# Kernel tuning notes

Measured on AMD Instinct MI355X. Metric: run time of the kernel, lower is better.

The kernel has to match this reference:

```python
import jax, jax.numpy as jnp
import numpy as np

T_Q, T_K, B, H, V = 32, 48, 64, 1024, 32320
MASK_FILL = -65504.0  # GNMT uses fp16 min


def setup_inputs() -> dict:
    key = jax.random.key(0)
    ks = jax.random.split(key, 12)
    s = 0.02
    inp = {
        "input1": jax.random.normal(ks[0], (T_K, B, H), jnp.float32),
        "input0": jax.random.normal(ks[1], (T_K, B, H), jnp.float32),
        "input2": jax.random.randint(ks[2], (B,), 1, T_K + 1),          # context lengths in [1, T_K]
        "input3": jax.random.randint(ks[3], (T_Q, B), 0, V),            # decoder token ids
        "emb": (jax.random.normal(ks[4], (V, H), jnp.float32) * 0.1).at[0].set(0.0),  # padding_idx=0
        "W_ih": jax.random.normal(ks[5], (4 * H, H), jnp.float32) * s,
        "W_hh": jax.random.normal(ks[6], (4 * H, H), jnp.float32) * s,
        "b_ih": jnp.zeros((4 * H,), jnp.float32),
        "b_hh": jnp.zeros((4 * H,), jnp.float32),
        "W_q": jax.random.normal(ks[7], (H, H), jnp.float32) * s,
        "W_k": jax.random.normal(ks[8], (H, H), jnp.float32) * s,
        "v_att": jax.random.normal(ks[9], (H,), jnp.float32) * s,
        "norm_scalar": jnp.array([1.0 / np.sqrt(H)], jnp.float32),
        "norm_bias": jnp.zeros((H,), jnp.float32),
    }
    return inp


def _lstm(x, W_ih, W_hh, b_ih, b_hh):
    # x: (T, B, In). PyTorch LSTM gate order: i, f, g, o. Zero initial state.
    xp = jnp.einsum('tbi,gi->tbg', x, W_ih) + b_ih + b_hh  # (T, B, 4H)
    Hh = W_hh.shape[1]

    def step(carry, xt):
        h, c = carry
        gates = xt + h @ W_hh.T
        i, f, g, o = jnp.split(gates, 4, axis=-1)
        c = jax.nn.sigmoid(f) * c + jax.nn.sigmoid(i) * jnp.tanh(g)
        h = jax.nn.sigmoid(o) * jnp.tanh(c)
        return (h, c), h

    h0 = jnp.zeros((x.shape[1], Hh), x.dtype)
    _, hs = jax.lax.scan(step, (h0, h0), xp)
    return hs  # (T, B, H)


def _forward(input1, input0, input2, input3, emb, W_ih, W_hh, b_ih, b_hh,
             W_q, W_k, v_att, norm_scalar, norm_bias):
    x = emb[input3]                       # (T_Q, B, H) embedding lookup
    ctx = input0 + input1                 # (T_K, B, H) residual-summed encoder context
    rnn_out = _lstm(x, W_ih, W_hh, b_ih, b_hh)   # (T_Q, B, H)

    # Bahdanau attention (batch_first=False -> transpose to batch-first)
    q = rnn_out.transpose(1, 0, 2)        # (B, T_Q, H)
    keys = ctx.transpose(1, 0, 2)         # (B, T_K, H)
    aq = q @ W_q.T                        # (B, T_Q, H)
    ak = keys @ W_k.T                     # (B, T_K, H)
    v = v_att / jnp.linalg.norm(v_att) * norm_scalar[0]  # normalized attention vector
    sum_qk = aq[:, :, None, :] + ak[:, None, :, :] + norm_bias  # (B, T_Q, T_K, H)
    scores = jnp.einsum('bqkh,h->bqk', jnp.tanh(sum_qk), v)
    pad = jnp.arange(T_K)[None, :] >= input2[:, None]            # (B, T_K), True = pad
    scores = jnp.where(pad[:, None, :], MASK_FILL, scores)
    attn = jax.nn.softmax(scores, axis=-1)
    context = jnp.einsum('bqk,bkh->bqh', attn, keys).transpose(1, 0, 2)  # (T_Q, B, H)
    # dropout p=0 -> identity; returns (rnn_outputs, attn_context) = (out12, out11)
    return rnn_out, context


def reference(input1, input0, input2, input3, emb, W_ih, W_hh, b_ih, b_hh,
              W_q, W_k, v_att, norm_scalar, norm_bias):
    return _forward(input1, input0, input2, input3, emb, W_ih, W_hh, b_ih, b_hh,
                    W_q, W_k, v_att, norm_scalar, norm_bias)
```

## Files before the change

kernel.cpp:

```cpp
#include <hip/hip_runtime.h>
#include <hip/hip_bf16.h>

typedef unsigned short u16;
typedef __attribute__((ext_vector_type(8))) short bf16x8;
typedef __attribute__((ext_vector_type(8))) unsigned short us8;
typedef __attribute__((ext_vector_type(4))) float f32x4;

#define T_Q 32
#define T_K 48
#define NB 64
#define HDIM 1024
#define MASK_FILL -65504.0f
#define LSTM_BLOCKS 64

__device__ __forceinline__ float bf2f(u16 v){
  union { unsigned u; float f; } x; x.u = ((unsigned)v) << 16; return x.f;
}
__device__ __forceinline__ u16 f2bf(float f){
  union { float f; unsigned u; } x; x.f = f;
  return (u16)((x.u + 0x7FFFu + ((x.u >> 16) & 1u)) >> 16);
}
__device__ __forceinline__ float sigm(float x){
  return __builtin_amdgcn_rcpf(1.f + __expf(-x));
}
__device__ __forceinline__ float tanh_f(float x){
  float e = __expf(2.f * x);
  return fmaf(-2.f, __builtin_amdgcn_rcpf(e + 1.f), 1.f);
}

__device__ __forceinline__ void st_b32_cc(u16* a, unsigned v){
  asm volatile("global_store_dword %0, %1, off sc0 sc1" :: "v"(a), "v"(v) : "memory");
}
__device__ __forceinline__ void st_flag(int* a, int v){
  asm volatile("global_store_dword %0, %1, off sc0 sc1" :: "v"(a), "v"(v) : "memory");
}
__device__ __forceinline__ int ld_flag(const int* a){
  int r;
  asm volatile("global_load_dword %0, %1, off sc0 sc1\n\ts_waitcnt vmcnt(0)"
               : "=v"(r) : "v"(a) : "memory");
  return r;
}

#define MFMA16(A,B,C) __builtin_amdgcn_mfma_f32_16x16x32_bf16(A,B,C,0,0,0)


__global__ void conv_f2b(const float* __restrict__ s, u16* __restrict__ d){
  size_t i = ((size_t)blockIdx.x * 256 + threadIdx.x) * 4;
  float4 v = *(const float4*)(s + i);
  ushort4 o; o.x = f2bf(v.x); o.y = f2bf(v.y); o.z = f2bf(v.z); o.w = f2bf(v.w);
  *(ushort4*)(d + i) = o;
}

__global__ void gather_x(const int* __restrict__ tok, const float* __restrict__ emb,
                         u16* __restrict__ x){
  int r = blockIdx.x;
  int token = tok[r];
  float4 v = ((const float4*)(emb + (size_t)token * HDIM))[threadIdx.x];
  ushort4 o; o.x = f2bf(v.x); o.y = f2bf(v.y); o.z = f2bf(v.z); o.w = f2bf(v.w);
  ((ushort4*)(x + (size_t)r * HDIM))[threadIdx.x] = o;
}

__global__ void make_keys(const float* __restrict__ a, const float* __restrict__ b,
                          u16* __restrict__ o){
  size_t i = ((size_t)blockIdx.x * 256 + threadIdx.x) * 4;
  float4 va = *(const float4*)(a + i);
  float4 vb = *(const float4*)(b + i);
  ushort4 vo;
  vo.x = f2bf(va.x + vb.x);
  vo.y = f2bf(va.y + vb.y);
  vo.z = f2bf(va.z + vb.z);
  vo.w = f2bf(va.w + vb.w);
  *(ushort4*)(o + i) = vo;
}

__global__ void prep_small(const float* __restrict__ vatt, const float* __restrict__ ns,
                           const float* __restrict__ nb,
                           float* __restrict__ vhat, float* __restrict__ nbias){
  __shared__ float wred[4];
  int t = threadIdx.x, lane = t & 63, w = t >> 6;
  float vv[4]; float s = 0.f;
  #pragma unroll
  for (int j = 0; j < 4; j++){ vv[j] = vatt[t*4 + j]; s += vv[j]*vv[j]; }
  #pragma unroll
  for (int m = 32; m >= 1; m >>= 1) s += __shfl_xor(s, m);
  if (lane == 0) wred[w] = s;
  __syncthreads();
  float tot = wred[0] + wred[1] + wred[2] + wred[3];
  float scale = ns[0] / sqrtf(tot);
  #pragma unroll
  for (int j = 0; j < 4; j++) vhat[t*4 + j] = vv[j] * scale;
  #pragma unroll
  for (int j = 0; j < 4; j++){ int i = t + 256*j; nbias[i] = nb[i]; }
}

__global__ void prep_bsum(const float* __restrict__ bih, const float* __restrict__ bhh,
                          float* __restrict__ bias_sum){
  int i = blockIdx.x * 256 + threadIdx.x;
  bias_sum[i] = bih[i] + bhh[i];
}


template<int OB>
__global__ __launch_bounds__(256) void gemm_bf16(
  const u16* __restrict__ A, const u16* __restrict__ W,
  const float* __restrict__ bias, void* __restrict__ Cv,
  int M, int N, int K)
{
  __shared__ __align__(16) u16 As[4][66][8];
  __shared__ __align__(16) u16 Bs[4][66][8];
  const int t = threadIdx.x;
  const int m0 = blockIdx.y * 64, n0 = blockIdx.x * 64;
  const int lane = t & 63, w = t >> 6;
  const int wm = (w >> 1) * 32, wn = (w & 1) * 32;
  const int lr = lane & 15, g = lane >> 4;
  const int lrow = t >> 2, lkc = t & 3;
  f32x4 acc00 = {0,0,0,0}, acc01 = {0,0,0,0}, acc10 = {0,0,0,0}, acc11 = {0,0,0,0};
  const u16* aptr = A + (size_t)(m0 + lrow) * K + lkc * 8;
  const u16* wptr = W + (size_t)(n0 + lrow) * K + lkc * 8;
  for (int k0 = 0; k0 < K; k0 += 32){
    *(bf16x8*)(&As[lkc][lrow][0]) = *(const bf16x8*)(aptr + k0);
    *(bf16x8*)(&Bs[lkc][lrow][0]) = *(const bf16x8*)(wptr + k0);
    __syncthreads();
    bf16x8 a0 = *(const bf16x8*)(&As[g][wm      + lr][0]);
    bf16x8 a1 = *(const bf16x8*)(&As[g][wm + 16 + lr][0]);
    bf16x8 b0 = *(const bf16x8*)(&Bs[g][wn      + lr][0]);
    bf16x8 b1 = *(const bf16x8*)(&Bs[g][wn + 16 + lr][0]);
    acc00 = MFMA16(a0, b0, acc00);
    acc01 = MFMA16(a0, b1, acc01);
    acc10 = MFMA16(a1, b0, acc10);
    acc11 = MFMA16(a1, b1, acc11);
    __syncthreads();
  }
  const int rb = m0 + wm + g * 4;
  const int cb = n0 + wn + lr;
  float bv0 = bias ? bias[cb]      : 0.f;
  float bv1 = bias ? bias[cb + 16] : 0.f;
  #pragma unroll
  for (int r = 0; r < 4; r++){
    float v00 = acc00[r] + bv0, v01 = acc01[r] + bv1;
    float v10 = acc10[r] + bv0, v11 = acc11[r] + bv1;
    if (OB){
      u16* C = (u16*)Cv;
      C[(size_t)(rb + r)      * N + cb]      = f2bf(v00);
      C[(size_t)(rb + r)      * N + cb + 16] = f2bf(v01);
      C[(size_t)(rb + 16 + r) * N + cb]      = f2bf(v10);
      C[(size_t)(rb + 16 + r) * N + cb + 16] = f2bf(v11);
    } else {
      float* C = (float*)Cv;
      C[(size_t)(rb + r)      * N + cb]      = v00;
      C[(size_t)(rb + r)      * N + cb + 16] = v01;
      C[(size_t)(rb + 16 + r) * N + cb]      = v10;
      C[(size_t)(rb + 16 + r) * N + cb + 16] = v11;
    }
  }
}


__global__ __launch_bounds__(512, 1) void lstm_persistent(
  const float* __restrict__ Whh, const u16* __restrict__ xp,
  u16* __restrict__ hsteps,
  u16* __restrict__ qbuf, float* __restrict__ out0,
  int* __restrict__ flags)
{
  extern __shared__ char smem[];
  u16*  wlds = (u16*)smem;
  float* gl  = (float*)(smem + 131072);

  const int tid = threadIdx.x;
  const int c0 = blockIdx.x * 16;
  const int lane = tid & 63, w = tid >> 6;
  const int gate = w & 3, msub = w >> 2;
  const int lr = lane & 15, g = lane >> 4;

  #pragma unroll
  for (int i = 0; i < 16; i++){
    int e = (i * 512 + tid) * 8;
    int R = e >> 10, k = e & 1023;
    int gg = R >> 4, rr = R & 15, tt = k >> 5, kk = k & 31;
    const float* src = Whh + (size_t)((gg << 10) + c0 + rr) * 1024 + k;
    float4 v0 = *(const float4*)(src);
    float4 v1 = *(const float4*)(src + 4);
    u16* dst = wlds + (((gg * 32 + tt) * 16 + rr) * 32 + kk);
    ushort4 o0, o1;
    o0.x = f2bf(v0.x); o0.y = f2bf(v0.y); o0.z = f2bf(v0.z); o0.w = f2bf(v0.w);
    o1.x = f2bf(v1.x); o1.y = f2bf(v1.y); o1.z = f2bf(v1.z); o1.w = f2bf(v1.w);
    *(ushort4*)dst = o0; *(ushort4*)(dst + 4) = o1;
  }
  __syncthreads();

  const int pb = (tid * 2) >> 4;
  const int pc = (tid * 2) & 15;
  float c_state0 = 0.f, c_state1 = 0.f;

  const int arow = msub * 32 + lr;
  const int jc = g >> 1;
  const int cc = (g & 1) * 8;

  #pragma unroll 1
  for (int step = 0; step < T_Q; step++){
    f32x4 acc0 = {0,0,0,0}, acc1 = {0,0,0,0};

    if (step > 0){
      if (w == 0){
        const int* fp = flags + lane * 16;
        for (;;){
          int f = ld_flag(fp);
          if (__ballot(f >= step) == ~0ull) break;
          __builtin_amdgcn_s_sleep(1);
        }
      }
      __syncthreads();

      const u16* hb = hsteps + (size_t)(step - 1) * 65536;
      const u16* pa0 = hb + (size_t)jc * 1024 + (size_t)arow * 16 + cc;
      const u16* pa1 = pa0 + 16 * 16;
      bf16x8 a0[8], a1[8];
      #pragma unroll
      for (int p = 0; p < 8; p++){
        a0[p] = *(const bf16x8*)(pa0 + p * 2048);
        a1[p] = *(const bf16x8*)(pa1 + p * 2048);
      }
      #pragma unroll
      for (int t = 0; t < 32; t++){
        bf16x8 bfr = *(const bf16x8*)(wlds + ((size_t)(gate * 32 + t) * 16 + lr) * 32 + g * 8);
        acc0 = MFMA16(a0[t & 7], bfr, acc0);
        acc1 = MFMA16(a1[t & 7], bfr, acc1);
        if (t < 24){
          a0[t & 7] = *(const bf16x8*)(pa0 + (t + 8) * 2048);
          a1[t & 7] = *(const bf16x8*)(pa1 + (t + 8) * 2048);
        }
      }
    }

    const u16* xr = xp + ((size_t)(step * NB + pb)) * 4096 + c0 + pc;
    unsigned xw0 = *(const unsigned*)(xr);
    unsigned xw1 = *(const unsigned*)(xr + 1024);
    unsigned xw2 = *(const unsigned*)(xr + 2048);
    unsigned xw3 = *(const unsigned*)(xr + 3072);

    #pragma unroll
    for (int r = 0; r < 4; r++){
      gl[(gate * 64 + msub * 32 +      g * 4 + r) * 16 + lr] = acc0[r];
      gl[(gate * 64 + msub * 32 + 16 + g * 4 + r) * 16 + lr] = acc1[r];
    }
    __syncthreads();

    float hout0, hout1; u16 hb0, hb1;
    {
      float ig = gl[(0 * 64 + pb) * 16 + pc] + bf2f((u16)(xw0 & 0xFFFF));
      float fg = gl[(1 * 64 + pb) * 16 + pc] + bf2f((u16)(xw1 & 0xFFFF));
      float gg = gl[(2 * 64 + pb) * 16 + pc] + bf2f((u16)(xw2 & 0xFFFF));
      float og = gl[(3 * 64 + pb) * 16 + pc] + bf2f((u16)(xw3 & 0xFFFF));
      float cn = sigm(fg) * c_state0 + sigm(ig) * tanh_f(gg);
      c_state0 = cn;
      hout0 = sigm(og) * tanh_f(cn); hb0 = f2bf(hout0);
    }
    {
      float ig = gl[(0 * 64 + pb) * 16 + pc + 1] + bf2f((u16)(xw0 >> 16));
      float fg = gl[(1 * 64 + pb) * 16 + pc + 1] + bf2f((u16)(xw1 >> 16));
      float gg = gl[(2 * 64 + pb) * 16 + pc + 1] + bf2f((u16)(xw2 >> 16));
      float og = gl[(3 * 64 + pb) * 16 + pc + 1] + bf2f((u16)(xw3 >> 16));
      float cn = sigm(fg) * c_state1 + sigm(ig) * tanh_f(gg);
      c_state1 = cn;
      hout1 = sigm(og) * tanh_f(cn); hb1 = f2bf(hout1);
    }

    if (step < T_Q - 1){
      u16* hw = hsteps + (size_t)step * 65536 + (size_t)blockIdx.x * 1024 + pb * 16 + pc;
      unsigned hpack = (unsigned)hb0 | ((unsigned)hb1 << 16);
      st_b32_cc(hw, hpack);
      asm volatile("s_waitcnt vmcnt(0)" ::: "memory");
      __syncthreads();
      if (tid == 0) st_flag(flags + blockIdx.x * 16, step + 1);
    }

    ushort2 hh; hh.x = hb0; hh.y = hb1;
    *(ushort2*)(qbuf + ((size_t)pb * T_Q + step) * HDIM + c0 + pc) = hh;
    float2 ho; ho.x = hout0; ho.y = hout1;
    *(float2*)(out0 + ((size_t)(step * NB + pb)) * HDIM + c0 + pc) = ho;
  }
}


__global__ __launch_bounds__(256) void attn_fused(
  const float* __restrict__ aq, const u16* __restrict__ ak,
  const float* __restrict__ vhat, const u16* __restrict__ keys,
  const int* __restrict__ lens, float* __restrict__ out1)
{
  int b = blockIdx.x >> 5, q = blockIdx.x & 31;
  int t = threadIdx.x, lane = t & 63, w = t >> 6;
  __shared__ float sc[T_K];
  __shared__ float ps[T_K];
  int len = lens[b];
  float aqr[16], vh[16];
  const float* aqp = aq + (size_t)(b * T_Q + q) * HDIM + lane * 16;
  const float* vp  = vhat + lane * 16;
  #pragma unroll
  for (int j = 0; j < 4; j++){
    float4 v0 = ((const float4*)aqp)[j];
    float4 v1 = ((const float4*)vp)[j];
    aqr[j*4+0] = v0.x; aqr[j*4+1] = v0.y; aqr[j*4+2] = v0.z; aqr[j*4+3] = v0.w;
    vh[j*4+0]  = v1.x; vh[j*4+1]  = v1.y; vh[j*4+2]  = v1.z; vh[j*4+3]  = v1.w;
  }

  int kmax = len - w * 12; if (kmax > 12) kmax = 12;
  for (int kk = 0; kk < kmax; kk++){
    int k = w * 12 + kk;
    const u16* akp = ak + (size_t)(k * NB + b) * HDIM + lane * 16;
    us8 a0 = *(const us8*)(akp);
    us8 a1 = *(const us8*)(akp + 8);
    float p = 0.f;
    #pragma unroll
    for (int j = 0; j < 8; j++){
      p += tanh_f(aqr[j]     + bf2f(a0[j])) * vh[j];
      p += tanh_f(aqr[8 + j] + bf2f(a1[j])) * vh[8 + j];
    }
    #pragma unroll
    for (int m = 32; m >= 1; m >>= 1) p += __shfl_xor(p, m);
    if (lane == 0) sc[k] = p;
  }
  __syncthreads();
  float mx = -3.0e38f;
  for (int k = 0; k < len; k++) mx = fmaxf(mx, sc[k]);
  if (t < len) ps[t] = __expf(sc[t] - mx);
  __syncthreads();
  float den = 0.f;
  for (int k = 0; k < len; k++) den += ps[k];
  float rden = __builtin_amdgcn_rcpf(den);

  float c0 = 0.f, c1 = 0.f, c2 = 0.f, c3 = 0.f;
  for (int k = 0; k < len; k++){
    float pk = ps[k];
    ushort4 kv = *(const ushort4*)(keys + (size_t)(k * NB + b) * HDIM + t * 4);
    c0 += pk * bf2f(kv.x); c1 += pk * bf2f(kv.y);
    c2 += pk * bf2f(kv.z); c3 += pk * bf2f(kv.w);
  }
  size_t o = (size_t)(q * NB + b) * HDIM + t * 4;
  out1[o + 0] = c0 * rden;
  out1[o + 1] = c1 * rden;
  out1[o + 2] = c2 * rden;
  out1[o + 3] = c3 * rden;
}


extern "C" void kernel_launch(void* const* d_in, const int* in_sizes, int n_in,
                              void* d_out, int out_size, void* d_ws, size_t ws_size,
                              hipStream_t stream)
{
  const float* in1  = (const float*)d_in[0];
  const float* in0  = (const float*)d_in[1];
  const int*   lens = (const int*)d_in[2];
  const int*   toks = (const int*)d_in[3];
  const float* emb  = (const float*)d_in[4];
  const float* Wih  = (const float*)d_in[5];
  const float* Whh  = (const float*)d_in[6];
  const float* bih  = (const float*)d_in[7];
  const float* bhh  = (const float*)d_in[8];
  const float* Wq   = (const float*)d_in[9];
  const float* Wk   = (const float*)d_in[10];
  const float* vatt = (const float*)d_in[11];
  const float* ns   = (const float*)d_in[12];
  const float* nbb  = (const float*)d_in[13];

  char* p = (char*)d_ws;
  u16* x_bf    = (u16*)p;   p += (size_t)2048 * 1024 * 2;
  u16* keys_bf = (u16*)p;   p += (size_t)3072 * 1024 * 2;
  u16* hsteps  = (u16*)p;   p += (size_t)32 * 65536 * 2;
  u16* qbuf    = (u16*)p;   p += (size_t)2048 * 1024 * 2;
  u16* xp      = (u16*)p;   p += (size_t)2048 * 4096 * 2;
  float* vhat  = (float*)p; p += 1024 * 4;
  float* bsum  = (float*)p; p += 4096 * 4;
  float* nbf   = (float*)p; p += 1024 * 4;
  int* flags   = (int*)p;   p += 4096;
  u16* ak      = (u16*)p;   p += (size_t)3072 * 1024 * 2;
  u16* Wih_bf  = (u16*)p;   p += (size_t)4096 * 1024 * 2;
  u16* Wq_bf   = (u16*)p;   p += (size_t)1024 * 1024 * 2;
  u16* Wk_bf   = (u16*)p;   p += (size_t)1024 * 1024 * 2;
  float* aq    = (float*)xp;

  float* out0 = (float*)d_out;
  float* out1 = out0 + (size_t)T_Q * NB * HDIM;

  hipMemsetAsync(flags, 0, 4096, stream);

  conv_f2b<<<4096, 256, 0, stream>>>(Wih, Wih_bf);
  conv_f2b<<<1024, 256, 0, stream>>>(Wq,  Wq_bf);
  conv_f2b<<<1024, 256, 0, stream>>>(Wk,  Wk_bf);
  gather_x<<<2048, 256, 0, stream>>>(toks, emb, x_bf);
  make_keys<<<3072, 256, 0, stream>>>(in1, in0, keys_bf);
  prep_small<<<1, 256, 0, stream>>>(vatt, ns, nbb, vhat, nbf);
  prep_bsum<<<16, 256, 0, stream>>>(bih, bhh, bsum);

  gemm_bf16<1><<<dim3(64, 32), 256, 0, stream>>>(x_bf, Wih_bf, bsum, xp, 2048, 4096, 1024);
  gemm_bf16<1><<<dim3(16, 48), 256, 0, stream>>>(keys_bf, Wk_bf, nbf, ak, 3072, 1024, 1024);

  lstm_persistent<<<LSTM_BLOCKS, 512, 147456, stream>>>(Whh, xp, hsteps, qbuf, out0, flags);

  gemm_bf16<0><<<dim3(16, 32), 256, 0, stream>>>(qbuf, Wq_bf, nullptr, aq, 2048, 1024, 1024);

  attn_fused<<<2048, 256, 0, stream>>>(aq, ak, vhat, keys_bf, lens, out1);
}
```

Before: 337.8 us.

## Replace global barrier wait with per-chunk flag polling overlapped with MFMA consumption

Each wave now polls the producer flags for one group of 8 blocks at a time and starts the matching slice of the recurrent h·W_hh product as soon as that group has published, instead of wave 0 waiting for all 64 blocks and then a __syncthreads. The intent is to overlap the tail of the inter-block dependency wait with MFMA work and to drop the block-wide barrier. The accumulators are split into two chains to shorten MFMA dependency chains, and the x-projection loads are hoisted ahead of the wait. The cost is that every wave now polls global flags, with the sleep removed, which adds memory traffic, and the loads are less deeply prefetched than the previous 8-deep pipeline.

```diff
diff --git a/kernel.cpp b/kernel.cpp
--- a/kernel.cpp
+++ b/kernel.cpp
@@ -198,45 +198,56 @@
 
   #pragma unroll 1
   for (int step = 0; step < T_Q; step++){
-    f32x4 acc0 = {0,0,0,0}, acc1 = {0,0,0,0};
-
-    if (step > 0){
-      if (w == 0){
-        const int* fp = flags + lane * 16;
-        for (;;){
-          int f = ld_flag(fp);
-          if (__ballot(f >= step) == ~0ull) break;
-          __builtin_amdgcn_s_sleep(1);
-        }
-      }
-      __syncthreads();
-
-      const u16* hb = hsteps + (size_t)(step - 1) * 65536;
-      const u16* pa0 = hb + (size_t)jc * 1024 + (size_t)arow * 16 + cc;
-      const u16* pa1 = pa0 + 16 * 16;
-      bf16x8 a0[8], a1[8];
-      #pragma unroll
-      for (int p = 0; p < 8; p++){
-        a0[p] = *(const bf16x8*)(pa0 + p * 2048);
-        a1[p] = *(const bf16x8*)(pa1 + p * 2048);
-      }
-      #pragma unroll
-      for (int t = 0; t < 32; t++){
-        bf16x8 bfr = *(const bf16x8*)(wlds + ((size_t)(gate * 32 + t) * 16 + lr) * 32 + g * 8);
-        acc0 = MFMA16(a0[t & 7], bfr, acc0);
-        acc1 = MFMA16(a1[t & 7], bfr, acc1);
-        if (t < 24){
-          a0[t & 7] = *(const bf16x8*)(pa0 + (t + 8) * 2048);
-          a1[t & 7] = *(const bf16x8*)(pa1 + (t + 8) * 2048);
-        }
-      }
-    }
-
     const u16* xr = xp + ((size_t)(step * NB + pb)) * 4096 + c0 + pc;
     unsigned xw0 = *(const unsigned*)(xr);
     unsigned xw1 = *(const unsigned*)(xr + 1024);
     unsigned xw2 = *(const unsigned*)(xr + 2048);
     unsigned xw3 = *(const unsigned*)(xr + 3072);
+
+    f32x4 acc0a = {0,0,0,0}, acc0b = {0,0,0,0};
+    f32x4 acc1a = {0,0,0,0}, acc1b = {0,0,0,0};
+
+    if (step > 0){
+      const u16* hb  = hsteps + (size_t)(step - 1) * 65536;
+      const u16* pa0 = hb + (size_t)jc * 1024 + (size_t)arow * 16 + cc;
+      const u16* pa1 = pa0 + 256;
+
+      auto consume = [&](int gq){
+        const u16* A0 = pa0 + gq * 8192;
+        const u16* A1 = pa1 + gq * 8192;
+        bf16x8 a00 = *(const bf16x8*)(A0);
+        bf16x8 a01 = *(const bf16x8*)(A0 + 2048);
+        bf16x8 a02 = *(const bf16x8*)(A0 + 4096);
+        bf16x8 a03 = *(const bf16x8*)(A0 + 6144);
+        bf16x8 a10 = *(const bf16x8*)(A1);
+        bf16x8 a11 = *(const bf16x8*)(A1 + 2048);
+        bf16x8 a12 = *(const bf16x8*)(A1 + 4096);
+        bf16x8 a13 = *(const bf16x8*)(A1 + 6144);
+        const u16* wb = wlds + ((size_t)(gate * 32 + gq * 4) * 16 + lr) * 32 + g * 8;
+        bf16x8 b0 = *(const bf16x8*)(wb);
+        bf16x8 b1 = *(const bf16x8*)(wb + 512);
+        bf16x8 b2 = *(const bf16x8*)(wb + 1024);
+        bf16x8 b3 = *(const bf16x8*)(wb + 1536);
+        acc0a = MFMA16(a00, b0, acc0a); acc1a = MFMA16(a10, b0, acc1a);
+        acc0b = MFMA16(a01, b1, acc0b); acc1b = MFMA16(a11, b1, acc1b);
+        acc0a = MFMA16(a02, b2, acc0a); acc1a = MFMA16(a12, b2, acc1a);
+        acc0b = MFMA16(a03, b3, acc0b); acc1b = MFMA16(a13, b3, acc1b);
+      };
+
+      #pragma unroll 1
+      for (int gq = 0; gq < 8; gq++){
+        const int* fpg = flags + ((gq * 8 + (lane & 7)) << 4);
+        for (;;){
+          int f = ld_flag(fpg);
+          if (__ballot(f >= step) == ~0ull) break;
+        }
+        __builtin_amdgcn_sched_barrier(0);
+        consume(gq);
+      }
+    }
+    f32x4 acc0, acc1;
+    #pragma unroll
+    for (int r = 0; r < 4; r++){ acc0[r] = acc0a[r] + acc0b[r]; acc1[r] = acc1a[r] + acc1b[r]; }
 
     #pragma unroll
     for (int r = 0; r < 4; r++){
```

Result: slower. 510.7 us (+51.2%).

## Use 128x128 GEMM tiles with 4x4 MFMA per wave; prefetch xp in LSTM

Applied to the files above, without the earlier changes.

The bf16 GEMM is retiled from 64x64 to 128x128 output blocks. Each wave now computes a 64x64 sub-tile with 16 MFMAs per k-step, which raises arithmetic intensity and cuts global and LDS traffic per flop. The cost is more register pressure from 16 accumulators and fewer blocks: 128 or 192, against 256 compute units. The LDS layout is also changed to row-major [128][32], which may cause bank conflicts. In the LSTM step loop, the xp input loads are moved ahead of the flag spin-wait so their latency overlaps the wait.

```diff
diff --git a/kernel.cpp b/kernel.cpp
--- a/kernel.cpp
+++ b/kernel.cpp
@@ -101,56 +101,69 @@
 
 
 template<int OB>
-__global__ __launch_bounds__(256) void gemm_bf16(
+__global__ __launch_bounds__(256) void gemm128(
   const u16* __restrict__ A, const u16* __restrict__ W,
   const float* __restrict__ bias, void* __restrict__ Cv,
   int M, int N, int K)
 {
-  __shared__ __align__(16) u16 As[4][66][8];
-  __shared__ __align__(16) u16 Bs[4][66][8];
+  __shared__ __align__(16) u16 As[128][32];
+  __shared__ __align__(16) u16 Bs[128][32];
   const int t = threadIdx.x;
-  const int m0 = blockIdx.y * 64, n0 = blockIdx.x * 64;
+  const int m0 = blockIdx.y * 128, n0 = blockIdx.x * 128;
   const int lane = t & 63, w = t >> 6;
-  const int wm = (w >> 1) * 32, wn = (w & 1) * 32;
+  const int wm = (w >> 1) * 64, wn = (w & 1) * 64;
   const int lr = lane & 15, g = lane >> 4;
-  const int lrow = t >> 2, lkc = t & 3;
-  f32x4 acc00 = {0,0,0,0}, acc01 = {0,0,0,0}, acc10 = {0,0,0,0}, acc11 = {0,0,0,0};
-  const u16* aptr = A + (size_t)(m0 + lrow) * K + lkc * 8;
-  const u16* wptr = W + (size_t)(n0 + lrow) * K + lkc * 8;
+  const int srow = t >> 2, skc = t & 3;
+
+  f32x4 acc[4][4];
+  #pragma unroll
+  for (int i = 0; i < 4; i++)
+    #pragma unroll
+    for (int j = 0; j < 4; j++) acc[i][j] = (f32x4){0,0,0,0};
+
+  const u16* aptr0 = A + (size_t)(m0 + srow)      * K + skc * 8;
+  const u16* aptr1 = A + (size_t)(m0 + 64 + srow) * K + skc * 8;
+  const u16* wptr0 = W + (size_t)(n0 + srow)      * K + skc * 8;
+  const u16* wptr1 = W + (size_t)(n0 + 64 + srow) * K + skc * 8;
+
   for (int k0 = 0; k0 < K; k0 += 32){
-    *(bf16x8*)(&As[lkc][lrow][0]) = *(const bf16x8*)(aptr + k0);
-    *(bf16x8*)(&Bs[lkc][lrow][0]) = *(const bf16x8*)(wptr + k0);
+    bf16x8 va0 = *(const bf16x8*)(aptr0 + k0);
+    bf16x8 va1 = *(const bf16x8*)(aptr1 + k0);
+    bf16x8 vb0 = *(const bf16x8*)(wptr0 + k0);
+    bf16x8 vb1 = *(const bf16x8*)(wptr1 + k0);
+    *(bf16x8*)(&As[srow][skc * 8])      = va0;
+    *(bf16x8*)(&As[64 + srow][skc * 8]) = va1;
+    *(bf16x8*)(&Bs[srow][skc * 8])      = vb0;
+    *(bf16x8*)(&Bs[64 + srow][skc * 8]) = vb1;
     __syncthreads();
-    bf16x8 a0 = *(const bf16x8*)(&As[g][wm      + lr][0]);
-    bf16x8 a1 = *(const bf16x8*)(&As[g][wm + 16 + lr][0]);
-    bf16x8 b0 = *(const bf16x8*)(&Bs[g][wn      + lr][0]);
-    bf16x8 b1 = *(const bf16x8*)(&Bs[g][wn + 16 + lr][0]);
-    acc00 = MFMA16(a0, b0, acc00);
-    acc01 = MFMA16(a0, b1, acc01);
-    acc10 = MFMA16(a1, b0, acc10);
-    acc11 = MFMA16(a1, b1, acc11);
+    bf16x8 af[4], bfr[4];
+    #pragma unroll
+    for (int mi = 0; mi < 4; mi++) af[mi]  = *(const bf16x8*)(&As[wm + mi * 16 + lr][g * 8]);
+    #pragma unroll
+    for (int ni = 0; ni < 4; ni++) bfr[ni] = *(const bf16x8*)(&Bs[wn + ni * 16 + lr][g * 8]);
+    #pragma unroll
+    for (int mi = 0; mi < 4; mi++)
+      #pragma unroll
+      for (int ni = 0; ni < 4; ni++)
+        acc[mi][ni] = MFMA16(af[mi], bfr[ni], acc[mi][ni]);
     __syncthreads();
   }
-  const int rb = m0 + wm + g * 4;
-  const int cb = n0 + wn + lr;
-  float bv0 = bias ? bias[cb]      : 0.f;
-  float bv1 = bias ? bias[cb + 16] : 0.f;
-  #pragma unroll
-  for (int r = 0; r < 4; r++){
-    float v00 = acc00[r] + bv0, v01 = acc01[r] + bv1;
-    float v10 = acc10[r] + bv0, v11 = acc11[r] + bv1;
-    if (OB){
-      u16* C = (u16*)Cv;
-      C[(size_t)(rb + r)      * N + cb]      = f2bf(v00);
-      C[(size_t)(rb + r)      * N + cb + 16] = f2bf(v01);
-      C[(size_t)(rb + 16 + r) * N + cb]      = f2bf(v10);
-      C[(size_t)(rb + 16 + r) * N + cb + 16] = f2bf(v11);
-    } else {
-      float* C = (float*)Cv;
-      C[(size_t)(rb + r)      * N + cb]      = v00;
-      C[(size_t)(rb + r)      * N + cb + 16] = v01;
-      C[(size_t)(rb + 16 + r) * N + cb]      = v10;
-      C[(size_t)(rb + 16 + r) * N + cb + 16] = v11;
+
+  float bv[4];
+  #pragma unroll
+  for (int ni = 0; ni < 4; ni++) bv[ni] = bias ? bias[n0 + wn + ni * 16 + lr] : 0.f;
+  #pragma unroll
+  for (int mi = 0; mi < 4; mi++){
+    #pragma unroll
+    for (int r = 0; r < 4; r++){
+      const size_t row = (size_t)(m0 + wm + mi * 16 + g * 4 + r);
+      #pragma unroll
+      for (int ni = 0; ni < 4; ni++){
+        float v = acc[mi][ni][r] + bv[ni];
+        const size_t col = (size_t)(n0 + wn + ni * 16 + lr);
+        if (OB) ((u16*)Cv)[row * N + col] = f2bf(v);
+        else    ((float*)Cv)[row * N + col] = v;
+      }
     }
   }
 }
@@ -198,6 +211,12 @@
 
   #pragma unroll 1
   for (int step = 0; step < T_Q; step++){
+    const u16* xr = xp + ((size_t)(step * NB + pb)) * 4096 + c0 + pc;
+    unsigned xw0 = *(const unsigned*)(xr);
+    unsigned xw1 = *(const unsigned*)(xr + 1024);
+    unsigned xw2 = *(const unsigned*)(xr + 2048);
+    unsigned xw3 = *(const unsigned*)(xr + 3072);
+
     f32x4 acc0 = {0,0,0,0}, acc1 = {0,0,0,0};
 
     if (step > 0){
@@ -213,7 +232,7 @@
 
       const u16* hb = hsteps + (size_t)(step - 1) * 65536;
       const u16* pa0 = hb + (size_t)jc * 1024 + (size_t)arow * 16 + cc;
-      const u16* pa1 = pa0 + 16 * 16;
+      const u16* pa1 = pa0 + 256;
       bf16x8 a0[8], a1[8];
       #pragma unroll
       for (int p = 0; p < 8; p++){
@@ -231,12 +250,6 @@
         }
       }
     }
-
-    const u16* xr = xp + ((size_t)(step * NB + pb)) * 4096 + c0 + pc;
-    unsigned xw0 = *(const unsigned*)(xr);
-    unsigned xw1 = *(const unsigned*)(xr + 1024);
-    unsigned xw2 = *(const unsigned*)(xr + 2048);
-    unsigned xw3 = *(const unsigned*)(xr + 3072);
 
     #pragma unroll
     for (int r = 0; r < 4; r++){
@@ -391,12 +404,12 @@
   prep_small<<<1, 256, 0, stream>>>(vatt, ns, nbb, vhat, nbf);
   prep_bsum<<<16, 256, 0, stream>>>(bih, bhh, bsum);
 
-  gemm_bf16<1><<<dim3(64, 32), 256, 0, stream>>>(x_bf, Wih_bf, bsum, xp, 2048, 4096, 1024);
-  gemm_bf16<1><<<dim3(16, 48), 256, 0, stream>>>(keys_bf, Wk_bf, nbf, ak, 3072, 1024, 1024);
+  gemm128<1><<<dim3(32, 16), 256, 0, stream>>>(x_bf, Wih_bf, bsum, xp, 2048, 4096, 1024);
+  gemm128<1><<<dim3(8, 24), 256, 0, stream>>>(keys_bf, Wk_bf, nbf, ak, 3072, 1024, 1024);
 
   lstm_persistent<<<LSTM_BLOCKS, 512, 147456, stream>>>(Whh, xp, hsteps, qbuf, out0, flags);
 
-  gemm_bf16<0><<<dim3(16, 32), 256, 0, stream>>>(qbuf, Wq_bf, nullptr, aq, 2048, 1024, 1024);
+  gemm128<0><<<dim3(8, 16), 256, 0, stream>>>(qbuf, Wq_bf, nullptr, aq, 2048, 1024, 1024);
 
   attn_fused<<<2048, 256, 0, stream>>>(aq, ak, vhat, keys_bf, lens, out1);
 }
```

Result: slower. 347.4 us (+2.8%).

## Overlap LSTM recurrent wait with per-group readiness flags and pipelined K-chunks

Applied to the files above, without the earlier changes.

Replaces the all-blocks barrier at each LSTM step with per-group readiness. Wave 0 polls the 64 producer flags and publishes readiness for each group of 8 blocks into LDS. The other waves spin on the LDS flag for each K-chunk, then load and multiply it in a double-buffered pipeline, so MFMA work on early chunks overlaps waiting for slower producer blocks. The xp gate-input loads are also hoisted ahead of the wait. The cost is extra LDS spinning and more complex synchronisation that relies on LDS volatile ordering instead of a __syncthreads.

```diff
diff --git a/kernel.cpp b/kernel.cpp
--- a/kernel.cpp
+++ b/kernel.cpp
@@ -165,12 +165,15 @@
   extern __shared__ char smem[];
   u16*  wlds = (u16*)smem;
   float* gl  = (float*)(smem + 131072);
+  volatile int* lds_ready = (volatile int*)(smem + 147456);
 
   const int tid = threadIdx.x;
   const int c0 = blockIdx.x * 16;
   const int lane = tid & 63, w = tid >> 6;
   const int gate = w & 3, msub = w >> 2;
   const int lr = lane & 15, g = lane >> 4;
+
+  if (tid < 8) lds_ready[tid] = 0;
 
   #pragma unroll
   for (int i = 0; i < 16; i++){
@@ -196,47 +199,72 @@
   const int jc = g >> 1;
   const int cc = (g & 1) * 8;
 
+#define SPING(gq) \
+  do { while (lds_ready[gq] < step) __builtin_amdgcn_s_sleep(1); \
+       asm volatile("" ::: "memory"); } while (0)
+
+#define LOADG(s0, s1, gq) \
+  do { const u16* A0_ = pa0 + (gq) * 8192; const u16* A1_ = pa1 + (gq) * 8192; \
+       s0[0] = *(const bf16x8*)(A0_);        s1[0] = *(const bf16x8*)(A1_); \
+       s0[1] = *(const bf16x8*)(A0_ + 2048); s1[1] = *(const bf16x8*)(A1_ + 2048); \
+       s0[2] = *(const bf16x8*)(A0_ + 4096); s1[2] = *(const bf16x8*)(A1_ + 4096); \
+       s0[3] = *(const bf16x8*)(A0_ + 6144); s1[3] = *(const bf16x8*)(A1_ + 6144); } while (0)
+
+#define MFMAG(s0, s1, gq) \
+  do { const u16* wb_ = wlds + ((size_t)(gate * 32 + (gq) * 4) * 16 + lr) * 32 + g * 8; \
+       bf16x8 b0_ = *(const bf16x8*)(wb_); \
+       bf16x8 b1_ = *(const bf16x8*)(wb_ + 512); \
+       bf16x8 b2_ = *(const bf16x8*)(wb_ + 1024); \
+       bf16x8 b3_ = *(const bf16x8*)(wb_ + 1536); \
+       acc0 = MFMA16(s0[0], b0_, acc0); acc1 = MFMA16(s1[0], b0_, acc1); \
+       acc0 = MFMA16(s0[1], b1_, acc0); acc1 = MFMA16(s1[1], b1_, acc1); \
+       acc0 = MFMA16(s0[2], b2_, acc0); acc1 = MFMA16(s1[2], b2_, acc1); \
+       acc0 = MFMA16(s0[3], b3_, acc0); acc1 = MFMA16(s1[3], b3_, acc1); } while (0)
+
   #pragma unroll 1
   for (int step = 0; step < T_Q; step++){
-    f32x4 acc0 = {0,0,0,0}, acc1 = {0,0,0,0};
-
-    if (step > 0){
-      if (w == 0){
-        const int* fp = flags + lane * 16;
-        for (;;){
-          int f = ld_flag(fp);
-          if (__ballot(f >= step) == ~0ull) break;
-          __builtin_amdgcn_s_sleep(1);
-        }
-      }
-      __syncthreads();
-
-      const u16* hb = hsteps + (size_t)(step - 1) * 65536;
-      const u16* pa0 = hb + (size_t)jc * 1024 + (size_t)arow * 16 + cc;
-      const u16* pa1 = pa0 + 16 * 16;
-      bf16x8 a0[8], a1[8];
-      #pragma unroll
-      for (int p = 0; p < 8; p++){
-        a0[p] = *(const bf16x8*)(pa0 + p * 2048);
-        a1[p] = *(const bf16x8*)(pa1 + p * 2048);
-      }
-      #pragma unroll
-      for (int t = 0; t < 32; t++){
-        bf16x8 bfr = *(const bf16x8*)(wlds + ((size_t)(gate * 32 + t) * 16 + lr) * 32 + g * 8);
-        acc0 = MFMA16(a0[t & 7], bfr, acc0);
-        acc1 = MFMA16(a1[t & 7], bfr, acc1);
-        if (t < 24){
-          a0[t & 7] = *(const bf16x8*)(pa0 + (t + 8) * 2048);
-          a1[t & 7] = *(const bf16x8*)(pa1 + (t + 8) * 2048);
-        }
-      }
-    }
-
     const u16* xr = xp + ((size_t)(step * NB + pb)) * 4096 + c0 + pc;
     unsigned xw0 = *(const unsigned*)(xr);
     unsigned xw1 = *(const unsigned*)(xr + 1024);
     unsigned xw2 = *(const unsigned*)(xr + 2048);
     unsigned xw3 = *(const unsigned*)(xr + 3072);
+
+    f32x4 acc0 = {0,0,0,0}, acc1 = {0,0,0,0};
+
+    if (step > 0){
+      if (w == 0){
+        unsigned done = 0;
+        const int* fp = flags + lane * 16;
+        while (done != 0xFFu){
+          int f = ld_flag(fp);
+          unsigned long long b = __ballot(f >= step);
+          #pragma unroll
+          for (int gq = 0; gq < 8; gq++){
+            if (((done >> gq) & 1u) == 0 &&
+                ((unsigned)(b >> (gq * 8)) & 0xFFu) == 0xFFu){
+              if (lane == 0) lds_ready[gq] = step;
+              done |= 1u << gq;
+            }
+          }
+          if (done != 0xFFu) __builtin_amdgcn_s_sleep(1);
+        }
+      }
+
+      const u16* hb  = hsteps + (size_t)(step - 1) * 65536;
+      const u16* pa0 = hb + (size_t)jc * 1024 + (size_t)arow * 16 + cc;
+      const u16* pa1 = pa0 + 256;
+
+      bf16x8 sA0[4], sA1[4], sB0[4], sB1[4];
+      SPING(0); LOADG(sA0, sA1, 0);
+      SPING(1); LOADG(sB0, sB1, 1); MFMAG(sA0, sA1, 0);
+      SPING(2); LOADG(sA0, sA1, 2); MFMAG(sB0, sB1, 1);
+      SPING(3); LOADG(sB0, sB1, 3); MFMAG(sA0, sA1, 2);
+      SPING(4); LOADG(sA0, sA1, 4); MFMAG(sB0, sB1, 3);
+      SPING(5); LOADG(sB0, sB1, 5); MFMAG(sA0, sA1, 4);
+      SPING(6); LOADG(sA0, sA1, 6); MFMAG(sB0, sB1, 5);
+      SPING(7); LOADG(sB0, sB1, 7); MFMAG(sA0, sA1, 6);
+      MFMAG(sB0, sB1, 7);
+    }
 
     #pragma unroll
     for (int r = 0; r < 4; r++){
@@ -279,6 +307,9 @@
     float2 ho; ho.x = hout0; ho.y = hout1;
     *(float2*)(out0 + ((size_t)(step * NB + pb)) * HDIM + c0 + pc) = ho;
   }
+#undef SPING
+#undef LOADG
+#undef MFMAG
 }
 
 
@@ -394,7 +425,7 @@
   gemm_bf16<1><<<dim3(64, 32), 256, 0, stream>>>(x_bf, Wih_bf, bsum, xp, 2048, 4096, 1024);
   gemm_bf16<1><<<dim3(16, 48), 256, 0, stream>>>(keys_bf, Wk_bf, nbf, ak, 3072, 1024, 1024);
 
-  lstm_persistent<<<LSTM_BLOCKS, 512, 147456, stream>>>(Whh, xp, hsteps, qbuf, out0, flags);
+  lstm_persistent<<<LSTM_BLOCKS, 512, 147488, stream>>>(Whh, xp, hsteps, qbuf, out0, flags);
 
   gemm_bf16<0><<<dim3(16, 32), 256, 0, stream>>>(qbuf, Wq_bf, nullptr, aq, 2048, 1024, 1024);
 
```

After: 333.3 us. Within noise of the previous version (-1.3%).
